# Performance work log

Hardware: AMD Instinct MI355X
Metric: run time of the kernel (lower is better)

Reference implementation:

```python
import jax, jax.numpy as jnp
import numpy as np

B, T, L, IN, D, H = 2, 16, 256, 768, 1024, 16
HD = D // H
NREG = 4
P = NREG + 2          # frozen prefix: registers + noise + action
DEPTH = 8
TINT = 4              # temporal_attention_interval
CTX = 30              # temporal_context_length
BASE = 1000.0         # rope_base
EPS = 1e-6            # qk_norm_eps / rmsnorm eps
HID = 4096            # 4.0 * latent_dim
S = L + P             # tokens per frame


def _rms(x, w=None, eps=EPS):
    y = x * jax.lax.rsqrt(jnp.mean(x * x, axis=-1, keepdims=True) + eps)
    return y * w if w is not None else y


def _rope_cache(n, hd, base):
    inv = base ** (-jnp.arange(0, hd, 2, dtype=jnp.float32) / hd)
    ang = jnp.arange(n, dtype=jnp.float32)[:, None] * inv[None, :]  # [n, hd/2]
    return jnp.cos(ang), jnp.sin(ang)


def _apply_rope(x, cos, sin):
    x1, x2 = x[..., ::2], x[..., 1::2]
    return jnp.stack([x1 * cos - x2 * sin, x1 * sin + x2 * cos], axis=-1).reshape(x.shape)


def _attn(x, Wqkv, Wo, cos, sin, mask):
    # x: [..., S, D]; mask: bool, True = attend, broadcastable to [..., H, S, S]
    qkv = x @ Wqkv
    q, k, v = jnp.split(qkv, 3, axis=-1)
    heads = lambda t: t.reshape(t.shape[:-1] + (H, HD)).swapaxes(-2, -3)  # [..., H, S, HD]
    q, k, v = heads(q), heads(k), heads(v)
    q = _apply_rope(_rms(q), cos, sin)   # qk-norm then RoPE
    k = _apply_rope(_rms(k), cos, sin)
    s = jnp.einsum('...qd,...kd->...qk', q, k) / jnp.sqrt(jnp.float32(HD))
    s = jnp.where(mask, s, jnp.float32(-1e9))
    p = jax.nn.softmax(s, axis=-1) * mask.any(axis=-1, keepdims=True)  # zero rows with no allowed keys
    o = jnp.einsum('...qk,...kd->...qd', p, v)
    return o.swapaxes(-2, -3).reshape(x.shape) @ Wo


def _spatial_mask():
    m = np.zeros((S, S), bool)
    r, n, a, ls = NREG, NREG, NREG + 1, NREG + 2
    m[ls:, ls:] = True; m[ls:, n] = True; m[ls:, a] = True; m[ls:, :r] = True
    m[n, n] = True; m[a, a] = True
    m[:r, ls:] = True; m[:r, n] = True; m[:r, a] = True; m[:r, :r] = True
    return jnp.asarray(m)


def _temporal_mask(indep):
    m = jnp.tril(jnp.ones((T, T), bool), -1)  # strictly-past causal
    if CTX is not None and CTX < T:
        m = m & jnp.triu(m, -CTX)             # sliding context window
    m = jnp.broadcast_to(m, (B, T, T))
    m = jnp.where(indep[:, None, None], False, m)
    return m[:, None, None]  # [B,1,1,T,T] -> broadcasts over token pos and heads


def setup_inputs() -> dict:
    key = jax.random.key(0)
    ks = iter(jax.random.split(key, 40))
    g = lambda shape, s=0.02: jax.random.normal(next(ks), shape, jnp.float32) * s
    inp = {
        'noisy_latents': jax.random.normal(next(ks), (B, T, L, IN), jnp.float32),
        'noise_levels': jax.random.uniform(next(ks), (B, T), jnp.float32),
        'actions': jax.random.normal(next(ks), (B, T, 6), jnp.float32),
        'independent_frames_mask': jnp.zeros((B,), bool),
        'actions_mask': jnp.ones((B, T), bool),
        'W_in': g((IN, D)),
        'noise_w1': g((1, D)), 'noise_b1': jnp.zeros((D,), jnp.float32),
        'noise_w2': g((D, D)), 'noise_b2': jnp.zeros((D,), jnp.float32),
        'base_action_embed': g((D,)),
        'action_w': g((6, D)), 'action_b': jnp.zeros((D,), jnp.float32),
        'registers': g((NREG, D)),
        'ln1_w': jnp.ones((DEPTH, D), jnp.float32),
        'Wqkv_s': g((DEPTH, D, 3 * D)), 'Wo_s': g((DEPTH, D, D)),
        'lnt_w': jnp.ones((DEPTH, D), jnp.float32),
        'Wqkv_t': g((DEPTH, D, 3 * D)), 'Wo_t': g((DEPTH, D, D)),
        'ln2_w': jnp.ones((DEPTH, D), jnp.float32),
        'W1': g((DEPTH, D, HID)), 'W2': g((DEPTH, D, HID)), 'W3': g((DEPTH, HID, D)),
        'final_w': jnp.ones((D,), jnp.float32),
        'W_out': g((D, IN)), 'b_out': jnp.zeros((IN,), jnp.float32),
    }
    return inp


def reference(noisy_latents, noise_levels, actions, independent_frames_mask, actions_mask,
              W_in, noise_w1, noise_b1, noise_w2, noise_b2, base_action_embed,
              action_w, action_b, registers, ln1_w, Wqkv_s, Wo_s, lnt_w, Wqkv_t, Wo_t,
              ln2_w, W1, W2, W3, final_w, W_out, b_out):
    noisy_tokens = noisy_latents @ W_in                                   # [B,T,L,D]
    base = jnp.broadcast_to(base_action_embed, (B, T, 1, D))
    act = base + (actions @ action_w + action_b)[:, :, None, :]
    act = jnp.where(actions_mask[:, :, None, None], act, base)            # [B,T,1,D]
    nz = jax.nn.silu(noise_levels[..., None] @ noise_w1 + noise_b1) @ noise_w2 + noise_b2
    nz = nz[:, :, None, :]                                                # [B,T,1,D]
    reg = jnp.broadcast_to(registers, (B, T, NREG, D))
    x = jnp.concatenate([reg, nz, act, noisy_tokens], axis=2)             # [B,T,S,D]

    sp_mask = _spatial_mask()
    tm_mask = _temporal_mask(independent_frames_mask)
    sp_cos, sp_sin = _rope_cache(S, HD, BASE)
    tm_cos, tm_sin = _rope_cache(T, HD, BASE)
    keep_tok = (jnp.arange(S) >= P)[None, :, None, None]                  # zero temporal update on frozen prefix

    for i in range(DEPTH):
        h = _rms(x, ln1_w[i])
        x = x + _attn(h, Wqkv_s[i], Wo_s[i], sp_cos, sp_sin, sp_mask)
        if i % TINT == 0:
            ht = _rms(x, lnt_w[i]).transpose(0, 2, 1, 3)                  # [B,S,T,D]
            ot = _attn(ht, Wqkv_t[i], Wo_t[i], tm_cos, tm_sin, tm_mask)
            x = x + (ot * keep_tok).transpose(0, 2, 1, 3)
        h2 = _rms(x, ln2_w[i])
        x = x + (jax.nn.silu(h2 @ W1[i]) * (h2 @ W2[i])) @ W3[i]

    latents = _rms(x[..., P:, :], final_w)
    pred_clean_latents = latents @ W_out + b_out                          # [B,T,L,IN]
    return pred_clean_latents
```

## Files before the change

### kernel.cpp

```cpp
#include <hip/hip_runtime.h>
#include <cstdint>
#include <cstddef>

#define DEV __device__ __forceinline__

typedef __attribute__((ext_vector_type(8))) __bf16 bf16x8;
typedef __attribute__((ext_vector_type(4))) float f32x4;

#define NTOK   8384
#define NTOKP  8448
#define NLAT   8192

DEV float b2f(unsigned short u) {
  unsigned int x = ((unsigned int)u) << 16;
  return __builtin_bit_cast(float, x);
}
DEV unsigned short f2b(float f) {
  unsigned int x = __builtin_bit_cast(unsigned int, f);
  x += 0x7fffu + ((x >> 16) & 1u);
  return (unsigned short)(x >> 16);
}
DEV float wred_sum(float v) {
#pragma unroll
  for (int o = 32; o; o >>= 1) v += __shfl_xor(v, o);
  return v;
}
DEV bool mask_or(const void* p, int i) {
  return ((const unsigned char*)p)[i] != 0 || ((const int*)p)[i] != 0;
}
DEV bool mask_and(const void* p, int i) {
  return ((const unsigned char*)p)[i] != 0 && ((const int*)p)[i] != 0;
}


__global__ void conv_f2b(const float* __restrict__ in, unsigned short* __restrict__ out, int n4) {
  int i = blockIdx.x * 256 + threadIdx.x;
  if (i < n4) {
    float4 v = ((const float4*)in)[i];
    ushort4 o;
    o.x = f2b(v.x); o.y = f2b(v.y); o.z = f2b(v.z); o.w = f2b(v.w);
    ((ushort4*)out)[i] = o;
  }
}

__global__ void build_rope(float2* __restrict__ out, int npos) {
  int idx = blockIdx.x * 256 + threadIdx.x;
  if (idx >= npos * 32) return;
  int pos = idx >> 5, i = idx & 31;
  float inv = powf(1000.0f, -(float)(2 * i) * (1.0f / 64.0f));
  float ang = (float)pos * inv;
  float sv, cv;
  sincosf(ang, &sv, &cv);
  out[idx] = make_float2(cv, sv);
}

__global__ __launch_bounds__(256) void transpose_w(const float* __restrict__ in,
                                                   unsigned short* __restrict__ out,
                                                   int K, int N, int ostride) {
  __shared__ float tile[32][33];
  int kb = blockIdx.x * 32, nb = blockIdx.y * 32;
  int tx = threadIdx.x & 31, ty = threadIdx.x >> 5;
#pragma unroll
  for (int i = 0; i < 32; i += 8)
    tile[ty + i][tx] = in[(size_t)(kb + ty + i) * N + (nb + tx)];
  __syncthreads();
#pragma unroll
  for (int i = 0; i < 32; i += 8)
    out[(size_t)(nb + ty + i) * ostride + (kb + tx)] = f2b(tile[tx][ty + i]);
}

__global__ __launch_bounds__(256) void noise_h1(const float* __restrict__ nlvl,
                                                const float* __restrict__ w1,
                                                const float* __restrict__ b1,
                                                const float* __restrict__ b2,
                                                float* __restrict__ h1,
                                                float* __restrict__ nz) {
  int i = blockIdx.x * 256 + threadIdx.x;
  int bt = i >> 10, d = i & 1023;
  float v = nlvl[bt] * w1[d] + b1[d];
  h1[i] = v / (1.0f + expf(-v));
  nz[i] = b2[d];
}

__global__ __launch_bounds__(256) void noise_mm(const float* __restrict__ h1,
                                                const float* __restrict__ w2,
                                                float* __restrict__ nz) {
  __shared__ float hs[32][128];
  int kc = blockIdx.x >> 4, dpg = blockIdx.x & 15;
  int tid = threadIdx.x;
  int k0 = kc * 128;
  for (int idx = tid; idx < 32 * 128; idx += 256) {
    int bt = idx >> 7, k = idx & 127;
    hs[bt][k] = h1[bt * 1024 + k0 + k];
  }
  __syncthreads();
  int dp = dpg * 64 + (tid & 63);
  int bt0 = (tid >> 6) * 8;
  float acc[8] = {};
  for (int k = 0; k < 128; ++k) {
    float w = w2[(size_t)(k0 + k) * 1024 + dp];
#pragma unroll
    for (int j = 0; j < 8; ++j) acc[j] += hs[bt0 + j][k] * w;
  }
#pragma unroll
  for (int j = 0; j < 8; ++j) atomicAdd(&nz[(bt0 + j) * 1024 + dp], acc[j]);
}

__global__ void embed_special(float* __restrict__ x, const float* __restrict__ regs,
                              const float* __restrict__ nz, const float* __restrict__ base_emb,
                              const float* __restrict__ actions, const float* __restrict__ action_w,
                              const float* __restrict__ action_b,
                              const void* __restrict__ amask) {
  int bt = blockIdx.x, d = threadIdx.x;
  float* xr = x + (size_t)bt * 262 * 1024;
#pragma unroll
  for (int r = 0; r < 4; ++r) xr[r * 1024 + d] = regs[r * 1024 + d];
  xr[4 * 1024 + d] = nz[(size_t)bt * 1024 + d];
  float a = base_emb[d];
  if (mask_or(amask, bt)) {
    float s = action_b[d];
#pragma unroll
    for (int i = 0; i < 6; ++i) s += actions[bt * 6 + i] * action_w[i * 1024 + d];
    a += s;
  }
  xr[5 * 1024 + d] = a;
}

template <bool REMAP>
__global__ __launch_bounds__(256) void rms_k(const float* __restrict__ x,
                                             const float* __restrict__ w,
                                             unsigned short* __restrict__ out) {
  int m = blockIdx.x, tid = threadIdx.x;
  size_t src = REMAP ? ((size_t)(m >> 8) * 262 + 6 + (m & 255)) : (size_t)m;
  float4 v = ((const float4*)(x + src * 1024))[tid];
  float ss = v.x * v.x + v.y * v.y + v.z * v.z + v.w * v.w;
  ss = wred_sum(ss);
  __shared__ float sred[4];
  if ((tid & 63) == 0) sred[tid >> 6] = ss;
  __syncthreads();
  float tot = sred[0] + sred[1] + sred[2] + sred[3];
  float sc = rsqrtf(tot * (1.0f / 1024.0f) + 1e-6f);
  float4 wv = ((const float4*)w)[tid];
  ushort4 o;
  o.x = f2b(v.x * sc * wv.x); o.y = f2b(v.y * sc * wv.y);
  o.z = f2b(v.z * sc * wv.z); o.w = f2b(v.w * sc * wv.w);
  ((ushort4*)(out + (size_t)m * 1024))[tid] = o;
}

#define KSTR 72
#define VSTR 296
__global__ __launch_bounds__(256) void attn_spatial(const unsigned short* __restrict__ qkv,
                                                    unsigned short* __restrict__ o,
                                                    const float2* __restrict__ rope) {
  __shared__ unsigned short Ks[272 * KSTR];
  __shared__ unsigned short Vt[64 * VSTR];
  __shared__ unsigned short Ps[4][16 * VSTR];
  const int h = blockIdx.x & 15;
  const int bt = blockIdx.x >> 4;
  const int tid = threadIdx.x, wave = tid >> 6, lane = tid & 63;
  const size_t tb = (size_t)bt * 262;

  {
    const int d = lane;
#pragma unroll 1
    for (int pss = 0; pss < 17; ++pss) {
      const int t0 = (pss * 4 + wave) * 4;
      ushort4 vp;
      unsigned short* vpp = (unsigned short*)&vp;
#pragma unroll
      for (int j = 0; j < 4; ++j) {
        const int t = t0 + j;
        float kv = 0.f, vv = 0.f;
        if (t < 262) {
          const size_t rb = (tb + t) * 3072 + h * 64 + d;
          kv = b2f(qkv[rb + 1024]);
          vv = b2f(qkv[rb + 2048]);
        }
        float ss = wred_sum(kv * kv);
        kv *= rsqrtf(ss * (1.0f / 64.0f) + 1e-6f);
        float partner = __shfl_xor(kv, 1);
        const int tc = t < 262 ? t : 261;
        float2 cs = rope[tc * 32 + (d >> 1)];
        kv = ((d & 1) == 0) ? (kv * cs.x - partner * cs.y)
                            : (partner * cs.y + kv * cs.x);
        Ks[t * KSTR + d] = f2b(kv);
        vpp[j] = f2b(vv);
      }
      *(ushort4*)(&Vt[d * VSTR + t0]) = vp;
    }
    for (int idx = tid; idx < 64 * 24; idx += 256) {
      Vt[(idx / 24) * VSTR + 272 + (idx % 24)] = 0;
    }
    for (int idx = tid; idx < 4 * 16 * 34; idx += 256) {
      int w = idx / (16 * 34), r = (idx / 34) & 15, c = idx % 34;
      Ps[w][r * VSTR + 262 + c] = 0;
    }
  }
  __syncthreads();

  unsigned short* Pw = &Ps[wave][0];
  const int kcol = lane & 15;
  const int g8 = (lane >> 4) << 3;
  const int g4 = g8 >> 1;
  const int rq = (lane >> 4) << 2;

#pragma unroll 1
  for (int qc = wave; qc < 17; qc += 4) {
    const int q0 = qc * 16;
    const int qrow = q0 + kcol;
    const int grow = qrow < 262 ? qrow : 261;
    const unsigned short* qp = qkv + (tb + grow) * 3072 + h * 64 + g8;
    float qv[16];
    {
      ushort4 a = *(const ushort4*)qp, b = *(const ushort4*)(qp + 4);
      ushort4 c = *(const ushort4*)(qp + 32), e = *(const ushort4*)(qp + 36);
      qv[0] = b2f(a.x); qv[1] = b2f(a.y); qv[2] = b2f(a.z); qv[3] = b2f(a.w);
      qv[4] = b2f(b.x); qv[5] = b2f(b.y); qv[6] = b2f(b.z); qv[7] = b2f(b.w);
      qv[8] = b2f(c.x); qv[9] = b2f(c.y); qv[10] = b2f(c.z); qv[11] = b2f(c.w);
      qv[12] = b2f(e.x); qv[13] = b2f(e.y); qv[14] = b2f(e.z); qv[15] = b2f(e.w);
    }
    float ss = 0.f;
#pragma unroll
    for (int i = 0; i < 16; ++i) ss += qv[i] * qv[i];
    ss += __shfl_xor(ss, 16);
    ss += __shfl_xor(ss, 32);
    const float qsc = rsqrtf(ss * (1.0f / 64.0f) + 1e-6f);
    bf16x8 aq0, aq1;
    unsigned short* u0 = (unsigned short*)&aq0;
    unsigned short* u1 = (unsigned short*)&aq1;
#pragma unroll
    for (int i = 0; i < 4; ++i) {
      float2 cs0 = rope[grow * 32 + g4 + i];
      float a = qv[2 * i] * qsc, b = qv[2 * i + 1] * qsc;
      u0[2 * i] = f2b(a * cs0.x - b * cs0.y);
      u0[2 * i + 1] = f2b(a * cs0.y + b * cs0.x);
      float2 cs1 = rope[grow * 32 + 16 + g4 + i];
      float a1 = qv[8 + 2 * i] * qsc, b1 = qv[9 + 2 * i] * qsc;
      u1[2 * i] = f2b(a1 * cs1.x - b1 * cs1.y);
      u1[2 * i + 1] = f2b(a1 * cs1.y + b1 * cs1.x);
    }
    f32x4 sc[17];
#pragma unroll
    for (int kc = 0; kc < 17; ++kc) {
      const unsigned short* kb = &Ks[(kc * 16 + kcol) * KSTR + g8];
      f32x4 z = {};
      z = __builtin_amdgcn_mfma_f32_16x16x32_bf16(aq0, *(const bf16x8*)kb, z, 0, 0, 0);
      sc[kc] = __builtin_amdgcn_mfma_f32_16x16x32_bf16(aq1, *(const bf16x8*)(kb + 32), z, 0, 0, 0);
    }
#pragma unroll
    for (int kc = 0; kc < 17; ++kc) {
      const int k = kc * 16 + kcol;
#pragma unroll
      for (int j = 0; j < 4; ++j) {
        const int sq = q0 + rq + j;
        const bool valid = (k < 262) && ((sq != 4 && sq != 5) || (k == sq));
        sc[kc][j] = valid ? sc[kc][j] * 0.125f : -1e30f;
      }
    }
    float sm[4];
#pragma unroll
    for (int j = 0; j < 4; ++j) {
      float m = -1e30f;
#pragma unroll
      for (int kc = 0; kc < 17; ++kc) m = fmaxf(m, sc[kc][j]);
#pragma unroll
      for (int off = 1; off < 16; off <<= 1) m = fmaxf(m, __shfl_xor(m, off));
      float s = 0.f;
#pragma unroll
      for (int kc = 0; kc < 17; ++kc) {
        float e = expf(sc[kc][j] - m);
        sc[kc][j] = e;
        s += e;
      }
#pragma unroll
      for (int off = 1; off < 16; off <<= 1) s += __shfl_xor(s, off);
      sm[j] = 1.0f / s;
    }
#pragma unroll
    for (int kc = 0; kc < 17; ++kc) {
      const int k = kc * 16 + kcol;
#pragma unroll
      for (int j = 0; j < 4; ++j)
        Pw[(rq + j) * VSTR + k] = f2b(sc[kc][j] * sm[j]);
    }
    f32x4 oacc[4] = {};
#pragma unroll
    for (int tc = 0; tc < 9; ++tc) {
      const bf16x8 ap = *(const bf16x8*)(&Pw[kcol * VSTR + tc * 32 + g8]);
#pragma unroll
      for (int nt = 0; nt < 4; ++nt) {
        const bf16x8 bv = *(const bf16x8*)(&Vt[(nt * 16 + kcol) * VSTR + tc * 32 + g8]);
        oacc[nt] = __builtin_amdgcn_mfma_f32_16x16x32_bf16(ap, bv, oacc[nt], 0, 0, 0);
      }
    }
#pragma unroll
    for (int nt = 0; nt < 4; ++nt) {
#pragma unroll
      for (int j = 0; j < 4; ++j) {
        const int sq = q0 + rq + j;
        if (sq < 262)
          o[(tb + sq) * 1024 + h * 64 + nt * 16 + kcol] = f2b(oacc[nt][j]);
      }
    }
  }
}

__global__ __launch_bounds__(256) void attn_temporal(const unsigned short* __restrict__ qkv,
                                                     unsigned short* __restrict__ o,
                                                     const float2* __restrict__ rope,
                                                     const void* __restrict__ indep) {
  int gw = blockIdx.x * 4 + (threadIdx.x >> 6);
  int lane = threadIdx.x & 63;
  if (gw >= NTOK) return;
  int h = gw & 15;
  int s = (gw >> 4) % 262;
  int b = (gw >> 4) / 262;
  bool dead = (s < 6) || mask_and(indep, b);
  float q[16], kk[16], vv[16], out[16];
#pragma unroll
  for (int t = 0; t < 16; ++t) {
    out[t] = 0.f;
    if (!dead) {
      size_t off = ((size_t)((b * 16 + t) * 262 + s)) * 3072 + h * 64 + lane;
      q[t] = b2f(qkv[off]);
      kk[t] = b2f(qkv[off + 1024]);
      vv[t] = b2f(qkv[off + 2048]);
    }
  }
  if (!dead) {
#pragma unroll
    for (int t = 0; t < 16; ++t) {
      float sq_ = wred_sum(q[t] * q[t]);
      float qv = q[t] * rsqrtf(sq_ * (1.0f / 64.0f) + 1e-6f);
      float sk_ = wred_sum(kk[t] * kk[t]);
      float kv = kk[t] * rsqrtf(sk_ * (1.0f / 64.0f) + 1e-6f);
      float2 cs = rope[t * 32 + (lane >> 1)];
      float qp = __shfl_xor(qv, 1);
      float kp = __shfl_xor(kv, 1);
      q[t] = ((lane & 1) == 0) ? (qv * cs.x - qp * cs.y) : (qp * cs.y + qv * cs.x);
      kk[t] = ((lane & 1) == 0) ? (kv * cs.x - kp * cs.y) : (kp * cs.y + kv * cs.x);
    }
#pragma unroll
    for (int t = 1; t < 16; ++t) {
      float m = -1e30f, l = 0.f, acc = 0.f;
#pragma unroll
      for (int j = 0; j < t; ++j) {
        float pr = q[t] * kk[j];
#pragma unroll
        for (int o2 = 32; o2; o2 >>= 1) pr += __shfl_xor(pr, o2);
        pr *= 0.125f;
        float mn = fmaxf(m, pr);
        float cor = expf(m - mn);
        float e = expf(pr - mn);
        l = l * cor + e;
        acc = acc * cor + e * vv[j];
        m = mn;
      }
      out[t] = acc / l;
    }
  }
#pragma unroll
  for (int t = 0; t < 16; ++t) {
    size_t off = ((size_t)((b * 16 + t) * 262 + s)) * 1024 + h * 64 + lane;
    o[off] = f2b(out[t]);
  }
}

DEV void stage_tiles(const unsigned short* __restrict__ A, const unsigned short* __restrict__ Bw,
                     size_t arow0, size_t brow0, int K, int k0,
                     unsigned short* As, unsigned short* Bs, int wave, int lane) {
  const int srow = lane >> 2;
  const int scol = (lane & 3) * 8;
#pragma unroll
  for (int c = 0; c < 2; ++c) {
    const int chunk = wave * 2 + c;
    unsigned short* ga = const_cast<unsigned short*>(A + (arow0 + chunk * 16 + srow) * K + k0 + scol);
    unsigned short* gb = const_cast<unsigned short*>(Bw + (brow0 + chunk * 16 + srow) * K + k0 + scol);
    __builtin_amdgcn_global_load_lds((__attribute__((address_space(1))) void*)ga,
                                     (__attribute__((address_space(3))) void*)(As + chunk * 512),
                                     16, 0, 0);
    __builtin_amdgcn_global_load_lds((__attribute__((address_space(1))) void*)gb,
                                     (__attribute__((address_space(3))) void*)(Bs + chunk * 512),
                                     16, 0, 0);
  }
}

template <int EPI>
__global__ __launch_bounds__(256) void gemm_k(const unsigned short* __restrict__ A,
                                              const unsigned short* __restrict__ Bw,
                                              void* __restrict__ C,
                                              const float* __restrict__ aux,
                                              int Mvalid, int K, int ldc) {
  __shared__ unsigned short As[2][128 * 32];
  __shared__ unsigned short Bs[2][128 * 32];
  const int tid = threadIdx.x;
  const int wave = tid >> 6, lane = tid & 63;
  const int wm = wave >> 1, wn = wave & 1;
  const size_t arow0 = (size_t)blockIdx.x * 128;
  const size_t brow0 = (size_t)blockIdx.y * 128;

  f32x4 acc[4][4] = {};
  const int KT = K >> 5;

  stage_tiles(A, Bw, arow0, brow0, K, 0, As[0], Bs[0], wave, lane);
  __syncthreads();
  int buf = 0;
  for (int kt = 0; kt < KT; ++kt) {
    if (kt + 1 < KT)
      stage_tiles(A, Bw, arow0, brow0, K, (kt + 1) << 5, As[buf ^ 1], Bs[buf ^ 1], wave, lane);
    const int kk = (lane >> 4) * 8;
    const int rsel = lane & 15;
    bf16x8 af[4], bfr[4];
#pragma unroll
    for (int mt = 0; mt < 4; ++mt)
      af[mt] = *reinterpret_cast<const bf16x8*>(&As[buf][(wm * 64 + mt * 16 + rsel) * 32 + kk]);
#pragma unroll
    for (int nt = 0; nt < 4; ++nt)
      bfr[nt] = *reinterpret_cast<const bf16x8*>(&Bs[buf][(wn * 64 + nt * 16 + rsel) * 32 + kk]);
#pragma unroll
    for (int mt = 0; mt < 4; ++mt) {
#pragma unroll
      for (int nt = 0; nt < 4; ++nt)
        acc[mt][nt] = __builtin_amdgcn_mfma_f32_16x16x32_bf16(af[mt], bfr[nt], acc[mt][nt], 0, 0, 0);
    }
    __syncthreads();
    buf ^= 1;
  }

  const int row_base = blockIdx.x * 128 + wm * 64;
  const int col_base = blockIdx.y * 128 + wn * 64;
#pragma unroll
  for (int mt = 0; mt < 4; ++mt) {
#pragma unroll
    for (int nt = 0; nt < 4; ++nt) {
      const int col = col_base + nt * 16 + (lane & 15);
      const int r0 = row_base + mt * 16 + ((lane >> 4) << 2);
#pragma unroll
      for (int j = 0; j < 4; ++j) {
        const int row = r0 + j;
        float v = acc[mt][nt][j];
        if (EPI == 2) {
          float partner = __shfl_xor(v, 1);
          if (row < Mvalid && !(lane & 1)) {
            float sv = v / (1.0f + expf(-v));
            ((unsigned short*)C)[(size_t)row * ldc + (col >> 1)] = f2b(sv * partner);
          }
        } else if (row < Mvalid) {
          if (EPI == 0) {
            ((unsigned short*)C)[(size_t)row * ldc + col] = f2b(v);
          } else if (EPI == 1) {
            float* p = (float*)C + (size_t)row * ldc + col;
            *p += v;
          } else if (EPI == 3) {
            ((float*)C)[(size_t)row * ldc + col] = v + aux[col];
          } else if (EPI == 4) {
            ((float*)C)[(size_t)row * ldc + col] = v;
          } else if (EPI == 5) {
            int xr = (row >> 8) * 262 + 6 + (row & 255);
            ((float*)C)[(size_t)xr * ldc + col] = v;
          }
        }
      }
    }
  }
}

extern "C" void kernel_launch(void* const* d_in, const int* in_sizes, int n_in,
                              void* d_out, int out_size, void* d_ws, size_t ws_size,
                              hipStream_t stream) {
  const float* noisy = (const float*)d_in[0];
  const float* nlvl = (const float*)d_in[1];
  const float* actions = (const float*)d_in[2];
  const void* indep = d_in[3];
  const void* amask = d_in[4];
  const float* W_in = (const float*)d_in[5];
  const float* noise_w1 = (const float*)d_in[6];
  const float* noise_b1 = (const float*)d_in[7];
  const float* noise_w2 = (const float*)d_in[8];
  const float* noise_b2 = (const float*)d_in[9];
  const float* base_emb = (const float*)d_in[10];
  const float* action_w = (const float*)d_in[11];
  const float* action_b = (const float*)d_in[12];
  const float* registers = (const float*)d_in[13];
  const float* ln1_w = (const float*)d_in[14];
  const float* Wqkv_s = (const float*)d_in[15];
  const float* Wo_s = (const float*)d_in[16];
  const float* lnt_w = (const float*)d_in[17];
  const float* Wqkv_t = (const float*)d_in[18];
  const float* Wo_t = (const float*)d_in[19];
  const float* ln2_w = (const float*)d_in[20];
  const float* W1 = (const float*)d_in[21];
  const float* W2 = (const float*)d_in[22];
  const float* W3 = (const float*)d_in[23];
  const float* final_w = (const float*)d_in[24];
  const float* W_out = (const float*)d_in[25];
  const float* b_out = (const float*)d_in[26];

  char* p = (char*)d_ws;
  auto alloc = [&](size_t bytes) {
    char* r = p;
    p += (bytes + 255) & ~(size_t)255;
    return r;
  };
  float* X = (float*)alloc((size_t)NTOKP * 1024 * 4);
  unsigned short* HB = (unsigned short*)alloc((size_t)NTOKP * 1024 * 2);
  unsigned short* AO = (unsigned short*)alloc((size_t)NTOKP * 1024 * 2);
  char* SCR = alloc((size_t)NTOKP * 4096 * 2);
  unsigned short* QKV = (unsigned short*)SCR;
  unsigned short* G = (unsigned short*)SCR;
  unsigned short* NLB = (unsigned short*)SCR;
  float* NZ = (float*)alloc(32 * 1024 * 4);
  float* H1 = (float*)alloc(32 * 1024 * 4);
  float2* RSP = (float2*)alloc(262 * 32 * 8);
  float2* RTM = (float2*)alloc(16 * 32 * 8);
  unsigned short* WINT = (unsigned short*)alloc((size_t)1024 * 768 * 2);
  unsigned short* WQKVS = (unsigned short*)alloc((size_t)8 * 3072 * 1024 * 2);
  unsigned short* WOS = (unsigned short*)alloc((size_t)8 * 1024 * 1024 * 2);
  unsigned short* WQKVT = (unsigned short*)alloc((size_t)8 * 3072 * 1024 * 2);
  unsigned short* WOT = (unsigned short*)alloc((size_t)8 * 1024 * 1024 * 2);
  unsigned short* W12T = (unsigned short*)alloc((size_t)8 * 8192 * 1024 * 2);
  unsigned short* W3T = (unsigned short*)alloc((size_t)8 * 1024 * 4096 * 2);
  unsigned short* WOUTT = (unsigned short*)alloc((size_t)768 * 1024 * 2);

  auto tr = [&](const float* in, unsigned short* out, int K, int N, int ostride) {
    dim3 g(K / 32, N / 32);
    transpose_w<<<g, 256, 0, stream>>>(in, out, K, N, ostride);
  };
  tr(W_in, WINT, 768, 1024, 768);
  for (int i = 0; i < 8; ++i) {
    tr(Wqkv_s + (size_t)i * 1024 * 3072, WQKVS + (size_t)i * 3072 * 1024, 1024, 3072, 1024);
    tr(Wo_s + (size_t)i * 1024 * 1024, WOS + (size_t)i * 1024 * 1024, 1024, 1024, 1024);
    tr(Wqkv_t + (size_t)i * 1024 * 3072, WQKVT + (size_t)i * 3072 * 1024, 1024, 3072, 1024);
    tr(Wo_t + (size_t)i * 1024 * 1024, WOT + (size_t)i * 1024 * 1024, 1024, 1024, 1024);
    tr(W1 + (size_t)i * 1024 * 4096, W12T + (size_t)i * 8192 * 1024, 1024, 4096, 2048);
    tr(W2 + (size_t)i * 1024 * 4096, W12T + (size_t)i * 8192 * 1024 + 1024, 1024, 4096, 2048);
    tr(W3 + (size_t)i * 4096 * 1024, W3T + (size_t)i * 1024 * 4096, 4096, 1024, 4096);
  }
  tr(W_out, WOUTT, 1024, 768, 1024);

  build_rope<<<33, 256, 0, stream>>>(RSP, 262);
  build_rope<<<2, 256, 0, stream>>>(RTM, 16);
  conv_f2b<<<6144, 256, 0, stream>>>(noisy, NLB, (NLAT * 768) / 4);
  noise_h1<<<128, 256, 0, stream>>>(nlvl, noise_w1, noise_b1, noise_b2, H1, NZ);
  noise_mm<<<128, 256, 0, stream>>>(H1, noise_w2, NZ);
  embed_special<<<32, 1024, 0, stream>>>(X, registers, NZ, base_emb, actions, action_w, action_b, amask);
  {
    dim3 g(64, 8);
    gemm_k<5><<<g, 256, 0, stream>>>(NLB, WINT, X, nullptr, NLAT, 768, 1024);
  }

  for (int i = 0; i < 8; ++i) {
    rms_k<false><<<NTOK, 256, 0, stream>>>(X, ln1_w + i * 1024, HB);
    {
      dim3 g(66, 24);
      gemm_k<0><<<g, 256, 0, stream>>>(HB, WQKVS + (size_t)i * 3072 * 1024, QKV, nullptr, NTOK, 1024, 3072);
    }
    attn_spatial<<<512, 256, 0, stream>>>(QKV, AO, RSP);
    {
      dim3 g(66, 8);
      gemm_k<1><<<g, 256, 0, stream>>>(AO, WOS + (size_t)i * 1024 * 1024, X, nullptr, NTOK, 1024, 1024);
    }
    if ((i & 3) == 0) {
      rms_k<false><<<NTOK, 256, 0, stream>>>(X, lnt_w + i * 1024, HB);
      {
        dim3 g(66, 24);
        gemm_k<0><<<g, 256, 0, stream>>>(HB, WQKVT + (size_t)i * 3072 * 1024, QKV, nullptr, NTOK, 1024, 3072);
      }
      attn_temporal<<<2096, 256, 0, stream>>>(QKV, AO, RTM, indep);
      {
        dim3 g(66, 8);
        gemm_k<1><<<g, 256, 0, stream>>>(AO, WOT + (size_t)i * 1024 * 1024, X, nullptr, NTOK, 1024, 1024);
      }
    }
    rms_k<false><<<NTOK, 256, 0, stream>>>(X, ln2_w + i * 1024, HB);
    {
      dim3 g(66, 64);
      gemm_k<2><<<g, 256, 0, stream>>>(HB, W12T + (size_t)i * 8192 * 1024, G, nullptr, NTOK, 1024, 4096);
    }
    {
      dim3 g(66, 8);
      gemm_k<1><<<g, 256, 0, stream>>>(G, W3T + (size_t)i * 1024 * 4096, X, nullptr, NTOK, 4096, 1024);
    }
  }

  rms_k<true><<<NLAT, 256, 0, stream>>>(X, final_w, HB);
  {
    dim3 g(64, 6);
    gemm_k<3><<<g, 256, 0, stream>>>(HB, WOUTT, d_out, b_out, NLAT, 1024, 768);
  }
}
```

Before: 6.225 ms.

## Add 256x256-tile 4-stage pipelined GEMM for QKV and gated-MLP up projections

Adds a new GEMM kernel with 512 threads, 256x256 output tiles, a 4-deep LDS ring buffer filled by direct global-to-LDS loads, XOR-swizzled LDS layout, and XCD-aware workgroup remapping. It replaces the older 128-tile GEMM for the QKV projections and the fused W1/W2 SiLU-gate projection. The aim is more data reuse per tile and overlap of loads with MFMA work, using interleaved barriers and priority hints. In exchange it uses 128 KB of LDS per workgroup, so occupancy is low, and the larger tiles leave a padded tail on the 8384-row M dimension.

Measured after the change: 6.922 ms. 1.11x slower.

```diff
diff --git a/kernel.cpp b/kernel.cpp
--- a/kernel.cpp
+++ b/kernel.cpp
@@ -30,6 +30,11 @@
 }
 DEV bool mask_and(const void* p, int i) {
   return ((const unsigned char*)p)[i] != 0 && ((const int*)p)[i] != 0;
+}
+DEV void wgb() {
+  asm volatile("" ::: "memory");
+  __builtin_amdgcn_s_barrier();
+  asm volatile("" ::: "memory");
 }
 
 
@@ -458,6 +463,124 @@
           } else if (EPI == 5) {
             int xr = (row >> 8) * 262 + 6 + (row & 255);
             ((float*)C)[(size_t)xr * ldc + col] = v;
+          }
+        }
+      }
+    }
+  }
+}
+
+DEV void stage256(const unsigned short* __restrict__ G, size_t row0, int K, int kt,
+                  unsigned short* lds, int wid, int lane) {
+  const int r0 = lane >> 2;
+  const int csrc = (lane & 3) ^ (r0 & 3);
+#pragma unroll
+  for (int l = 0; l < 2; ++l) {
+    const int row = wid * 32 + l * 16 + r0;
+    unsigned short* g = const_cast<unsigned short*>(G + (row0 + row) * (size_t)K + kt * 32 + csrc * 8);
+    __builtin_amdgcn_global_load_lds((__attribute__((address_space(1))) void*)g,
+                                     (__attribute__((address_space(3))) void*)(lds + (wid * 2 + l) * 512),
+                                     16, 0, 0);
+  }
+}
+
+template <int EPI>
+__global__ __launch_bounds__(512) void gemm256_k(const unsigned short* __restrict__ A,
+                                                 const unsigned short* __restrict__ Bw,
+                                                 void* __restrict__ C,
+                                                 int Mvalid, int K, int ldc, int nbx) {
+  __shared__ unsigned short As[4][8192];
+  __shared__ unsigned short Bs[4][8192];
+  const int tid = threadIdx.x;
+  const int wid = tid >> 6, lane = tid & 63;
+  const int wm = wid >> 2, wn = wid & 3;
+  const int nwg = gridDim.x;
+  const int qq = nwg >> 3, rr = nwg & 7;
+  const int xcd = blockIdx.x & 7, idx = blockIdx.x >> 3;
+  const int wg = (xcd < rr ? xcd * (qq + 1) : rr * (qq + 1) + (xcd - rr) * qq) + idx;
+  const int bx = wg % nbx, by = wg / nbx;
+  const size_t arow0 = (size_t)bx * 256;
+  const size_t brow0 = (size_t)by * 256;
+  const int NT = K >> 5;
+
+  const int rsel = lane & 15;
+  const int physc = ((lane >> 4) ^ (lane & 3)) << 3;
+
+  f32x4 acc[8][4] = {};
+
+  stage256(A, arow0, K, 0, As[0], wid, lane);
+  stage256(Bw, brow0, K, 0, Bs[0], wid, lane);
+  stage256(A, arow0, K, 1, As[1], wid, lane);
+  stage256(Bw, brow0, K, 1, Bs[1], wid, lane);
+  stage256(A, arow0, K, 2, As[2], wid, lane);
+  stage256(Bw, brow0, K, 2, Bs[2], wid, lane);
+  asm volatile("s_waitcnt vmcnt(8)" ::: "memory");
+  wgb();
+
+#pragma unroll 1
+  for (int kt = 0; kt < NT; ++kt) {
+    unsigned short* as = As[kt & 3];
+    unsigned short* bs = Bs[kt & 3];
+    bf16x8 bfr[4], af[4];
+#pragma unroll
+    for (int nt = 0; nt < 4; ++nt)
+      bfr[nt] = *(const bf16x8*)(bs + (wn * 64 + nt * 16 + rsel) * 32 + physc);
+#pragma unroll
+    for (int mt = 0; mt < 4; ++mt)
+      af[mt] = *(const bf16x8*)(as + (wm * 128 + mt * 16 + rsel) * 32 + physc);
+    if (kt + 3 < NT) stage256(A, arow0, K, kt + 3, As[(kt + 3) & 3], wid, lane);
+    wgb();
+    __builtin_amdgcn_s_setprio(1);
+#pragma unroll
+    for (int mt = 0; mt < 4; ++mt)
+#pragma unroll
+      for (int nt = 0; nt < 4; ++nt)
+        acc[mt][nt] = __builtin_amdgcn_mfma_f32_16x16x32_bf16(af[mt], bfr[nt], acc[mt][nt], 0, 0, 0);
+    __builtin_amdgcn_s_setprio(0);
+    wgb();
+#pragma unroll
+    for (int mt = 0; mt < 4; ++mt)
+      af[mt] = *(const bf16x8*)(as + (wm * 128 + (mt + 4) * 16 + rsel) * 32 + physc);
+    if (kt + 3 < NT) stage256(Bw, brow0, K, kt + 3, Bs[(kt + 3) & 3], wid, lane);
+    wgb();
+    __builtin_amdgcn_s_setprio(1);
+#pragma unroll
+    for (int mt = 0; mt < 4; ++mt)
+#pragma unroll
+      for (int nt = 0; nt < 4; ++nt)
+        acc[mt + 4][nt] = __builtin_amdgcn_mfma_f32_16x16x32_bf16(af[mt], bfr[nt], acc[mt + 4][nt], 0, 0, 0);
+    __builtin_amdgcn_s_setprio(0);
+    if (kt + 3 < NT) {
+      asm volatile("s_waitcnt vmcnt(8)" ::: "memory");
+    } else if (kt + 2 < NT) {
+      asm volatile("s_waitcnt vmcnt(4)" ::: "memory");
+    } else if (kt + 1 < NT) {
+      asm volatile("s_waitcnt vmcnt(0)" ::: "memory");
+    }
+    wgb();
+  }
+
+  const int row_base = bx * 256 + wm * 128;
+  const int col_base = by * 256 + wn * 64;
+#pragma unroll
+  for (int mt = 0; mt < 8; ++mt) {
+#pragma unroll
+    for (int nt = 0; nt < 4; ++nt) {
+      const int col = col_base + nt * 16 + rsel;
+      const int r0 = row_base + mt * 16 + ((lane >> 4) << 2);
+#pragma unroll
+      for (int j = 0; j < 4; ++j) {
+        const int row = r0 + j;
+        float v = acc[mt][nt][j];
+        if (EPI == 2) {
+          float partner = __shfl_xor(v, 1);
+          if (row < Mvalid && !(lane & 1)) {
+            float sv = v / (1.0f + expf(-v));
+            ((unsigned short*)C)[(size_t)row * ldc + (col >> 1)] = f2b(sv * partner);
+          }
+        } else if (row < Mvalid) {
+          if (EPI == 0) {
+            ((unsigned short*)C)[(size_t)row * ldc + col] = f2b(v);
           }
         }
       }
@@ -551,10 +674,7 @@
 
   for (int i = 0; i < 8; ++i) {
     rms_k<false><<<NTOK, 256, 0, stream>>>(X, ln1_w + i * 1024, HB);
-    {
-      dim3 g(66, 24);
-      gemm_k<0><<<g, 256, 0, stream>>>(HB, WQKVS + (size_t)i * 3072 * 1024, QKV, nullptr, NTOK, 1024, 3072);
-    }
+    gemm256_k<0><<<33 * 12, 512, 0, stream>>>(HB, WQKVS + (size_t)i * 3072 * 1024, QKV, NTOK, 1024, 3072, 33);
     attn_spatial<<<512, 256, 0, stream>>>(QKV, AO, RSP);
     {
       dim3 g(66, 8);
@@ -562,10 +682,7 @@
     }
     if ((i & 3) == 0) {
       rms_k<false><<<NTOK, 256, 0, stream>>>(X, lnt_w + i * 1024, HB);
-      {
-        dim3 g(66, 24);
-        gemm_k<0><<<g, 256, 0, stream>>>(HB, WQKVT + (size_t)i * 3072 * 1024, QKV, nullptr, NTOK, 1024, 3072);
-      }
+      gemm256_k<0><<<33 * 12, 512, 0, stream>>>(HB, WQKVT + (size_t)i * 3072 * 1024, QKV, NTOK, 1024, 3072, 33);
       attn_temporal<<<2096, 256, 0, stream>>>(QKV, AO, RTM, indep);
       {
         dim3 g(66, 8);
@@ -573,10 +690,7 @@
       }
     }
     rms_k<false><<<NTOK, 256, 0, stream>>>(X, ln2_w + i * 1024, HB);
-    {
-      dim3 g(66, 64);
-      gemm_k<2><<<g, 256, 0, stream>>>(HB, W12T + (size_t)i * 8192 * 1024, G, nullptr, NTOK, 1024, 4096);
-    }
+    gemm256_k<2><<<33 * 32, 512, 0, stream>>>(HB, W12T + (size_t)i * 8192 * 1024, G, NTOK, 1024, 4096, 33);
     {
       dim3 g(66, 8);
       gemm_k<1><<<g, 256, 0, stream>>>(G, W3T + (size_t)i * 1024 * 4096, X, nullptr, NTOK, 4096, 1024);
```

## Triple-buffer GEMM LDS staging with swizzle and XCD-aware block remap

Applied to the files above, without the earlier changes.

Converts the GEMM main loop from a double buffer to a three-stage LDS pipeline, using explicit vmcnt waits and bare barriers so loads run two tiles ahead. It XOR-swizzles the LDS column placement to reduce bank conflicts on fragment reads. It also launches a 1D grid and remaps block IDs so consecutive tiles land on the same XCD, which should improve L2 reuse. In exchange it uses more LDS per block, which may lower occupancy, and it relies on hand-written waitcnt correctness.

Measured after the change: 6.771 ms. 1.09x slower.

```diff
diff --git a/kernel.cpp b/kernel.cpp
--- a/kernel.cpp
+++ b/kernel.cpp
@@ -30,6 +30,11 @@
 }
 DEV bool mask_and(const void* p, int i) {
   return ((const unsigned char*)p)[i] != 0 && ((const int*)p)[i] != 0;
+}
+DEV void wgb() {
+  asm volatile("" ::: "memory");
+  __builtin_amdgcn_s_barrier();
+  asm volatile("" ::: "memory");
 }
 
 
@@ -370,7 +375,7 @@
                      size_t arow0, size_t brow0, int K, int k0,
                      unsigned short* As, unsigned short* Bs, int wave, int lane) {
   const int srow = lane >> 2;
-  const int scol = (lane & 3) * 8;
+  const int scol = (((lane & 3) ^ ((lane >> 4) & 3))) * 8;
 #pragma unroll
   for (int c = 0; c < 2; ++c) {
     const int chunk = wave * 2 + c;
@@ -390,50 +395,70 @@
                                               const unsigned short* __restrict__ Bw,
                                               void* __restrict__ C,
                                               const float* __restrict__ aux,
-                                              int Mvalid, int K, int ldc) {
-  __shared__ unsigned short As[2][128 * 32];
-  __shared__ unsigned short Bs[2][128 * 32];
+                                              int Mvalid, int K, int ldc, int nbx) {
+  __shared__ unsigned short As[3][128 * 32];
+  __shared__ unsigned short Bs[3][128 * 32];
   const int tid = threadIdx.x;
   const int wave = tid >> 6, lane = tid & 63;
   const int wm = wave >> 1, wn = wave & 1;
-  const size_t arow0 = (size_t)blockIdx.x * 128;
-  const size_t brow0 = (size_t)blockIdx.y * 128;
+  const int nwg = gridDim.x;
+  const int q8 = nwg >> 3, r8 = nwg & 7;
+  const int xcd = blockIdx.x & 7, sub = blockIdx.x >> 3;
+  const int wg = (xcd < r8 ? xcd * (q8 + 1) : r8 * (q8 + 1) + (xcd - r8) * q8) + sub;
+  const int bx = wg % nbx, by = wg / nbx;
+  const size_t arow0 = (size_t)bx * 128;
+  const size_t brow0 = (size_t)by * 128;
 
   f32x4 acc[4][4] = {};
   const int KT = K >> 5;
 
   stage_tiles(A, Bw, arow0, brow0, K, 0, As[0], Bs[0], wave, lane);
-  __syncthreads();
-  int buf = 0;
+  stage_tiles(A, Bw, arow0, brow0, K, 32, As[1], Bs[1], wave, lane);
+  asm volatile("s_waitcnt vmcnt(4)" ::: "memory");
+  wgb();
+
+  unsigned short *pa0 = As[0], *pa1 = As[1], *pa2 = As[2];
+  unsigned short *pb0 = Bs[0], *pb1 = Bs[1], *pb2 = Bs[2];
+  const int rsel = lane & 15;
+  const int kk = (((lane >> 4) ^ ((lane >> 2) & 3)) << 3);
+
+#pragma unroll 1
   for (int kt = 0; kt < KT; ++kt) {
-    if (kt + 1 < KT)
-      stage_tiles(A, Bw, arow0, brow0, K, (kt + 1) << 5, As[buf ^ 1], Bs[buf ^ 1], wave, lane);
-    const int kk = (lane >> 4) * 8;
-    const int rsel = lane & 15;
+    if (kt + 2 < KT)
+      stage_tiles(A, Bw, arow0, brow0, K, (kt + 2) << 5, pa2, pb2, wave, lane);
     bf16x8 af[4], bfr[4];
 #pragma unroll
     for (int mt = 0; mt < 4; ++mt)
-      af[mt] = *reinterpret_cast<const bf16x8*>(&As[buf][(wm * 64 + mt * 16 + rsel) * 32 + kk]);
+      af[mt] = *(const bf16x8*)(pa0 + (wm * 64 + mt * 16 + rsel) * 32 + kk);
 #pragma unroll
     for (int nt = 0; nt < 4; ++nt)
-      bfr[nt] = *reinterpret_cast<const bf16x8*>(&Bs[buf][(wn * 64 + nt * 16 + rsel) * 32 + kk]);
+      bfr[nt] = *(const bf16x8*)(pb0 + (wn * 64 + nt * 16 + rsel) * 32 + kk);
 #pragma unroll
     for (int mt = 0; mt < 4; ++mt) {
 #pragma unroll
       for (int nt = 0; nt < 4; ++nt)
         acc[mt][nt] = __builtin_amdgcn_mfma_f32_16x16x32_bf16(af[mt], bfr[nt], acc[mt][nt], 0, 0, 0);
     }
-    __syncthreads();
-    buf ^= 1;
-  }
-
-  const int row_base = blockIdx.x * 128 + wm * 64;
-  const int col_base = blockIdx.y * 128 + wn * 64;
+    if (kt + 1 < KT) {
+      if (kt + 2 < KT) {
+        asm volatile("s_waitcnt vmcnt(4)" ::: "memory");
+      } else {
+        asm volatile("s_waitcnt vmcnt(0)" ::: "memory");
+      }
+      wgb();
+    }
+    unsigned short* t;
+    t = pa0; pa0 = pa1; pa1 = pa2; pa2 = t;
+    t = pb0; pb0 = pb1; pb1 = pb2; pb2 = t;
+  }
+
+  const int row_base = bx * 128 + wm * 64;
+  const int col_base = by * 128 + wn * 64;
 #pragma unroll
   for (int mt = 0; mt < 4; ++mt) {
 #pragma unroll
     for (int nt = 0; nt < 4; ++nt) {
-      const int col = col_base + nt * 16 + (lane & 15);
+      const int col = col_base + nt * 16 + rsel;
       const int r0 = row_base + mt * 16 + ((lane >> 4) << 2);
 #pragma unroll
       for (int j = 0; j < 4; ++j) {
@@ -544,48 +569,24 @@
   noise_h1<<<128, 256, 0, stream>>>(nlvl, noise_w1, noise_b1, noise_b2, H1, NZ);
   noise_mm<<<128, 256, 0, stream>>>(H1, noise_w2, NZ);
   embed_special<<<32, 1024, 0, stream>>>(X, registers, NZ, base_emb, actions, action_w, action_b, amask);
-  {
-    dim3 g(64, 8);
-    gemm_k<5><<<g, 256, 0, stream>>>(NLB, WINT, X, nullptr, NLAT, 768, 1024);
-  }
+  gemm_k<5><<<64 * 8, 256, 0, stream>>>(NLB, WINT, X, nullptr, NLAT, 768, 1024, 64);
 
   for (int i = 0; i < 8; ++i) {
     rms_k<false><<<NTOK, 256, 0, stream>>>(X, ln1_w + i * 1024, HB);
-    {
-      dim3 g(66, 24);
-      gemm_k<0><<<g, 256, 0, stream>>>(HB, WQKVS + (size_t)i * 3072 * 1024, QKV, nullptr, NTOK, 1024, 3072);
-    }
+    gemm_k<0><<<66 * 24, 256, 0, stream>>>(HB, WQKVS + (size_t)i * 3072 * 1024, QKV, nullptr, NTOK, 1024, 3072, 66);
     attn_spatial<<<512, 256, 0, stream>>>(QKV, AO, RSP);
-    {
-      dim3 g(66, 8);
-      gemm_k<1><<<g, 256, 0, stream>>>(AO, WOS + (size_t)i * 1024 * 1024, X, nullptr, NTOK, 1024, 1024);
-    }
+    gemm_k<1><<<66 * 8, 256, 0, stream>>>(AO, WOS + (size_t)i * 1024 * 1024, X, nullptr, NTOK, 1024, 1024, 66);
     if ((i & 3) == 0) {
       rms_k<false><<<NTOK, 256, 0, stream>>>(X, lnt_w + i * 1024, HB);
-      {
-        dim3 g(66, 24);
-        gemm_k<0><<<g, 256, 0, stream>>>(HB, WQKVT + (size_t)i * 3072 * 1024, QKV, nullptr, NTOK, 1024, 3072);
-      }
+      gemm_k<0><<<66 * 24, 256, 0, stream>>>(HB, WQKVT + (size_t)i * 3072 * 1024, QKV, nullptr, NTOK, 1024, 3072, 66);
       attn_temporal<<<2096, 256, 0, stream>>>(QKV, AO, RTM, indep);
-      {
-        dim3 g(66, 8);
-        gemm_k<1><<<g, 256, 0, stream>>>(AO, WOT + (size_t)i * 1024 * 1024, X, nullptr, NTOK, 1024, 1024);
-      }
+      gemm_k<1><<<66 * 8, 256, 0, stream>>>(AO, WOT + (size_t)i * 1024 * 1024, X, nullptr, NTOK, 1024, 1024, 66);
     }
     rms_k<false><<<NTOK, 256, 0, stream>>>(X, ln2_w + i * 1024, HB);
-    {
-      dim3 g(66, 64);
-      gemm_k<2><<<g, 256, 0, stream>>>(HB, W12T + (size_t)i * 8192 * 1024, G, nullptr, NTOK, 1024, 4096);
-    }
-    {
-      dim3 g(66, 8);
-      gemm_k<1><<<g, 256, 0, stream>>>(G, W3T + (size_t)i * 1024 * 4096, X, nullptr, NTOK, 4096, 1024);
-    }
+    gemm_k<2><<<66 * 64, 256, 0, stream>>>(HB, W12T + (size_t)i * 8192 * 1024, G, nullptr, NTOK, 1024, 4096, 66);
+    gemm_k<1><<<66 * 8, 256, 0, stream>>>(G, W3T + (size_t)i * 1024 * 4096, X, nullptr, NTOK, 4096, 1024, 66);
   }
 
   rms_k<true><<<NLAT, 256, 0, stream>>>(X, final_w, HB);
-  {
-    dim3 g(64, 6);
-    gemm_k<3><<<g, 256, 0, stream>>>(HB, WOUTT, d_out, b_out, NLAT, 1024, 768);
-  }
-}
+  gemm_k<3><<<64 * 6, 256, 0, stream>>>(HB, WOUTT, d_out, b_out, NLAT, 1024, 768, 64);
+}
```

## Split-K the N=1024 projection GEMMs with atomic accumulation and regroup SwiGLU weights

Applied to the files above, without the earlier changes.

The output-projection, W3 and final-output GEMMs are split in two along K using blockIdx.z, with float atomicAdd into the residual or output buffer. The final output gets a separate bias_fill pass first. This doubles the block count on grids that would otherwise fill the GPU poorly (66x8 tiles). Separately, W1 and W2 rows are interleaved in 16-row groups so the SwiGLU epilogue pairs accumulator tiles directly, with no cross-lane shuffle. The costs are atomic traffic on fp32 outputs, non-deterministic summation order and an extra fill kernel.

Measured after the change: 6.409 ms. 2.9% more time.

```diff
diff --git a/kernel.cpp b/kernel.cpp
--- a/kernel.cpp
+++ b/kernel.cpp
@@ -54,9 +54,14 @@
   out[idx] = make_float2(cv, sv);
 }
 
+__global__ void bias_fill(float* __restrict__ out, const float* __restrict__ b, int n) {
+  int i = blockIdx.x * 256 + threadIdx.x;
+  if (i < n) out[i] = b[i % 768];
+}
+
 __global__ __launch_bounds__(256) void transpose_w(const float* __restrict__ in,
                                                    unsigned short* __restrict__ out,
-                                                   int K, int N, int ostride) {
+                                                   int K, int N, int ostride, int mode) {
   __shared__ float tile[32][33];
   int kb = blockIdx.x * 32, nb = blockIdx.y * 32;
   int tx = threadIdx.x & 31, ty = threadIdx.x >> 5;
@@ -65,8 +70,13 @@
     tile[ty + i][tx] = in[(size_t)(kb + ty + i) * N + (nb + tx)];
   __syncthreads();
 #pragma unroll
-  for (int i = 0; i < 32; i += 8)
-    out[(size_t)(nb + ty + i) * ostride + (kb + tx)] = f2b(tile[tx][ty + i]);
+  for (int i = 0; i < 32; i += 8) {
+    int n = nb + ty + i;
+    int row = n;
+    if (mode == 1) row = ((n >> 4) << 5) | (n & 15);
+    else if (mode == 2) row = (((n >> 4) << 5) + 16) | (n & 15);
+    out[(size_t)row * ostride + (kb + tx)] = f2b(tile[tx][ty + i]);
+  }
 }
 
 __global__ __launch_bounds__(256) void noise_h1(const float* __restrict__ nlvl,
@@ -367,15 +377,15 @@
 }
 
 DEV void stage_tiles(const unsigned short* __restrict__ A, const unsigned short* __restrict__ Bw,
-                     size_t arow0, size_t brow0, int K, int k0,
+                     size_t arow0, size_t brow0, int lda, int k0,
                      unsigned short* As, unsigned short* Bs, int wave, int lane) {
   const int srow = lane >> 2;
   const int scol = (lane & 3) * 8;
 #pragma unroll
   for (int c = 0; c < 2; ++c) {
     const int chunk = wave * 2 + c;
-    unsigned short* ga = const_cast<unsigned short*>(A + (arow0 + chunk * 16 + srow) * K + k0 + scol);
-    unsigned short* gb = const_cast<unsigned short*>(Bw + (brow0 + chunk * 16 + srow) * K + k0 + scol);
+    unsigned short* ga = const_cast<unsigned short*>(A + (arow0 + chunk * 16 + srow) * lda + k0 + scol);
+    unsigned short* gb = const_cast<unsigned short*>(Bw + (brow0 + chunk * 16 + srow) * lda + k0 + scol);
     __builtin_amdgcn_global_load_lds((__attribute__((address_space(1))) void*)ga,
                                      (__attribute__((address_space(3))) void*)(As + chunk * 512),
                                      16, 0, 0);
@@ -390,7 +400,7 @@
                                               const unsigned short* __restrict__ Bw,
                                               void* __restrict__ C,
                                               const float* __restrict__ aux,
-                                              int Mvalid, int K, int ldc) {
+                                              int Mvalid, int K, int lda, int ldc) {
   __shared__ unsigned short As[2][128 * 32];
   __shared__ unsigned short Bs[2][128 * 32];
   const int tid = threadIdx.x;
@@ -398,16 +408,17 @@
   const int wm = wave >> 1, wn = wave & 1;
   const size_t arow0 = (size_t)blockIdx.x * 128;
   const size_t brow0 = (size_t)blockIdx.y * 128;
+  const int koff = blockIdx.z * K;
 
   f32x4 acc[4][4] = {};
   const int KT = K >> 5;
 
-  stage_tiles(A, Bw, arow0, brow0, K, 0, As[0], Bs[0], wave, lane);
+  stage_tiles(A, Bw, arow0, brow0, lda, koff, As[0], Bs[0], wave, lane);
   __syncthreads();
   int buf = 0;
   for (int kt = 0; kt < KT; ++kt) {
     if (kt + 1 < KT)
-      stage_tiles(A, Bw, arow0, brow0, K, (kt + 1) << 5, As[buf ^ 1], Bs[buf ^ 1], wave, lane);
+      stage_tiles(A, Bw, arow0, brow0, lda, koff + ((kt + 1) << 5), As[buf ^ 1], Bs[buf ^ 1], wave, lane);
     const int kk = (lane >> 4) * 8;
     const int rsel = lane & 15;
     bf16x8 af[4], bfr[4];
@@ -427,25 +438,44 @@
     buf ^= 1;
   }
 
+  const int rsel = lane & 15;
   const int row_base = blockIdx.x * 128 + wm * 64;
   const int col_base = blockIdx.y * 128 + wn * 64;
+
+  if (EPI == 2) {
+    const int cg0 = blockIdx.y * 64 + wn * 32;
+#pragma unroll
+    for (int mt = 0; mt < 4; ++mt) {
+#pragma unroll
+      for (int pr = 0; pr < 2; ++pr) {
+        const int col = cg0 + pr * 16 + rsel;
+        const int r0 = row_base + mt * 16 + ((lane >> 4) << 2);
+#pragma unroll
+        for (int j = 0; j < 4; ++j) {
+          const int row = r0 + j;
+          if (row < Mvalid) {
+            float u1 = acc[mt][pr * 2][j];
+            float u2 = acc[mt][pr * 2 + 1][j];
+            float sv = u1 / (1.0f + expf(-u1));
+            ((unsigned short*)C)[(size_t)row * ldc + col] = f2b(sv * u2);
+          }
+        }
+      }
+    }
+    return;
+  }
+
 #pragma unroll
   for (int mt = 0; mt < 4; ++mt) {
 #pragma unroll
     for (int nt = 0; nt < 4; ++nt) {
-      const int col = col_base + nt * 16 + (lane & 15);
+      const int col = col_base + nt * 16 + rsel;
       const int r0 = row_base + mt * 16 + ((lane >> 4) << 2);
 #pragma unroll
       for (int j = 0; j < 4; ++j) {
         const int row = r0 + j;
         float v = acc[mt][nt][j];
-        if (EPI == 2) {
-          float partner = __shfl_xor(v, 1);
-          if (row < Mvalid && !(lane & 1)) {
-            float sv = v / (1.0f + expf(-v));
-            ((unsigned short*)C)[(size_t)row * ldc + (col >> 1)] = f2b(sv * partner);
-          }
-        } else if (row < Mvalid) {
+        if (row < Mvalid) {
           if (EPI == 0) {
             ((unsigned short*)C)[(size_t)row * ldc + col] = f2b(v);
           } else if (EPI == 1) {
@@ -453,11 +483,11 @@
             *p += v;
           } else if (EPI == 3) {
             ((float*)C)[(size_t)row * ldc + col] = v + aux[col];
-          } else if (EPI == 4) {
-            ((float*)C)[(size_t)row * ldc + col] = v;
           } else if (EPI == 5) {
             int xr = (row >> 8) * 262 + 6 + (row & 255);
             ((float*)C)[(size_t)xr * ldc + col] = v;
+          } else if (EPI == 6) {
+            atomicAdd((float*)C + (size_t)row * ldc + col, v);
           }
         }
       }
@@ -522,21 +552,21 @@
   unsigned short* W3T = (unsigned short*)alloc((size_t)8 * 1024 * 4096 * 2);
   unsigned short* WOUTT = (unsigned short*)alloc((size_t)768 * 1024 * 2);
 
-  auto tr = [&](const float* in, unsigned short* out, int K, int N, int ostride) {
+  auto tr = [&](const float* in, unsigned short* out, int K, int N, int ostride, int mode) {
     dim3 g(K / 32, N / 32);
-    transpose_w<<<g, 256, 0, stream>>>(in, out, K, N, ostride);
+    transpose_w<<<g, 256, 0, stream>>>(in, out, K, N, ostride, mode);
   };
-  tr(W_in, WINT, 768, 1024, 768);
+  tr(W_in, WINT, 768, 1024, 768, 0);
   for (int i = 0; i < 8; ++i) {
-    tr(Wqkv_s + (size_t)i * 1024 * 3072, WQKVS + (size_t)i * 3072 * 1024, 1024, 3072, 1024);
-    tr(Wo_s + (size_t)i * 1024 * 1024, WOS + (size_t)i * 1024 * 1024, 1024, 1024, 1024);
-    tr(Wqkv_t + (size_t)i * 1024 * 3072, WQKVT + (size_t)i * 3072 * 1024, 1024, 3072, 1024);
-    tr(Wo_t + (size_t)i * 1024 * 1024, WOT + (size_t)i * 1024 * 1024, 1024, 1024, 1024);
-    tr(W1 + (size_t)i * 1024 * 4096, W12T + (size_t)i * 8192 * 1024, 1024, 4096, 2048);
-    tr(W2 + (size_t)i * 1024 * 4096, W12T + (size_t)i * 8192 * 1024 + 1024, 1024, 4096, 2048);
-    tr(W3 + (size_t)i * 4096 * 1024, W3T + (size_t)i * 1024 * 4096, 4096, 1024, 4096);
-  }
-  tr(W_out, WOUTT, 1024, 768, 1024);
+    tr(Wqkv_s + (size_t)i * 1024 * 3072, WQKVS + (size_t)i * 3072 * 1024, 1024, 3072, 1024, 0);
+    tr(Wo_s + (size_t)i * 1024 * 1024, WOS + (size_t)i * 1024 * 1024, 1024, 1024, 1024, 0);
+    tr(Wqkv_t + (size_t)i * 1024 * 3072, WQKVT + (size_t)i * 3072 * 1024, 1024, 3072, 1024, 0);
+    tr(Wo_t + (size_t)i * 1024 * 1024, WOT + (size_t)i * 1024 * 1024, 1024, 1024, 1024, 0);
+    tr(W1 + (size_t)i * 1024 * 4096, W12T + (size_t)i * 8192 * 1024, 1024, 4096, 1024, 1);
+    tr(W2 + (size_t)i * 1024 * 4096, W12T + (size_t)i * 8192 * 1024, 1024, 4096, 1024, 2);
+    tr(W3 + (size_t)i * 4096 * 1024, W3T + (size_t)i * 1024 * 4096, 4096, 1024, 4096, 0);
+  }
+  tr(W_out, WOUTT, 1024, 768, 1024, 0);
 
   build_rope<<<33, 256, 0, stream>>>(RSP, 262);
   build_rope<<<2, 256, 0, stream>>>(RTM, 16);
@@ -546,46 +576,47 @@
   embed_special<<<32, 1024, 0, stream>>>(X, registers, NZ, base_emb, actions, action_w, action_b, amask);
   {
     dim3 g(64, 8);
-    gemm_k<5><<<g, 256, 0, stream>>>(NLB, WINT, X, nullptr, NLAT, 768, 1024);
+    gemm_k<5><<<g, 256, 0, stream>>>(NLB, WINT, X, nullptr, NLAT, 768, 768, 1024);
   }
 
   for (int i = 0; i < 8; ++i) {
     rms_k<false><<<NTOK, 256, 0, stream>>>(X, ln1_w + i * 1024, HB);
     {
       dim3 g(66, 24);
-      gemm_k<0><<<g, 256, 0, stream>>>(HB, WQKVS + (size_t)i * 3072 * 1024, QKV, nullptr, NTOK, 1024, 3072);
+      gemm_k<0><<<g, 256, 0, stream>>>(HB, WQKVS + (size_t)i * 3072 * 1024, QKV, nullptr, NTOK, 1024, 1024, 3072);
     }
     attn_spatial<<<512, 256, 0, stream>>>(QKV, AO, RSP);
     {
-      dim3 g(66, 8);
-      gemm_k<1><<<g, 256, 0, stream>>>(AO, WOS + (size_t)i * 1024 * 1024, X, nullptr, NTOK, 1024, 1024);
+      dim3 g(66, 8, 2);
+      gemm_k<6><<<g, 256, 0, stream>>>(AO, WOS + (size_t)i * 1024 * 1024, X, nullptr, NTOK, 512, 1024, 1024);
     }
     if ((i & 3) == 0) {
       rms_k<false><<<NTOK, 256, 0, stream>>>(X, lnt_w + i * 1024, HB);
       {
         dim3 g(66, 24);
-        gemm_k<0><<<g, 256, 0, stream>>>(HB, WQKVT + (size_t)i * 3072 * 1024, QKV, nullptr, NTOK, 1024, 3072);
+        gemm_k<0><<<g, 256, 0, stream>>>(HB, WQKVT + (size_t)i * 3072 * 1024, QKV, nullptr, NTOK, 1024, 1024, 3072);
       }
       attn_temporal<<<2096, 256, 0, stream>>>(QKV, AO, RTM, indep);
       {
-        dim3 g(66, 8);
-        gemm_k<1><<<g, 256, 0, stream>>>(AO, WOT + (size_t)i * 1024 * 1024, X, nullptr, NTOK, 1024, 1024);
+        dim3 g(66, 8, 2);
+        gemm_k<6><<<g, 256, 0, stream>>>(AO, WOT + (size_t)i * 1024 * 1024, X, nullptr, NTOK, 512, 1024, 1024);
       }
     }
     rms_k<false><<<NTOK, 256, 0, stream>>>(X, ln2_w + i * 1024, HB);
     {
       dim3 g(66, 64);
-      gemm_k<2><<<g, 256, 0, stream>>>(HB, W12T + (size_t)i * 8192 * 1024, G, nullptr, NTOK, 1024, 4096);
+      gemm_k<2><<<g, 256, 0, stream>>>(HB, W12T + (size_t)i * 8192 * 1024, G, nullptr, NTOK, 1024, 1024, 4096);
     }
     {
-      dim3 g(66, 8);
-      gemm_k<1><<<g, 256, 0, stream>>>(G, W3T + (size_t)i * 1024 * 4096, X, nullptr, NTOK, 4096, 1024);
+      dim3 g(66, 8, 2);
+      gemm_k<6><<<g, 256, 0, stream>>>(G, W3T + (size_t)i * 1024 * 4096, X, nullptr, NTOK, 2048, 4096, 1024);
     }
   }
 
   rms_k<true><<<NLAT, 256, 0, stream>>>(X, final_w, HB);
+  bias_fill<<<24576, 256, 0, stream>>>((float*)d_out, b_out, NLAT * 768);
   {
-    dim3 g(64, 6);
-    gemm_k<3><<<g, 256, 0, stream>>>(HB, WOUTT, d_out, b_out, NLAT, 1024, 768);
-  }
-}
+    dim3 g(64, 6, 2);
+    gemm_k<6><<<g, 256, 0, stream>>>(HB, WOUTT, d_out, nullptr, NLAT, 512, 1024, 768);
+  }
+}
```
